# Kernel optimization log

Measured on AMD Instinct MI355X. Metric: run time of the kernel, lower is better.

Reference implementation:

```python
import jax, jax.numpy as jnp
import numpy as np

B = 65536   # batch
D = 48      # despawn feature dim (level*4)
T = 768     # transformer feature dim
F = 512     # fusion_dim
L = 64      # latent_dim
K = 2048    # num_embeddings
H = 4       # attention heads
COMMIT = 0.25


def _ln(x, w, b):
    m = x.mean(-1, keepdims=True)
    v = ((x - m) ** 2).mean(-1, keepdims=True)
    return (x - m) * jax.lax.rsqrt(v + 1e-5) * w + b


def _mha(q, k, v, in_w, in_b, out_w, out_b):
    # torch nn.MultiheadAttention (batch_first), q/k/v: [B, S, F]
    f = q.shape[-1]; dh = f // H
    wq, wk, wv = in_w[:f], in_w[f:2 * f], in_w[2 * f:]
    bq, bk, bv = in_b[:f], in_b[f:2 * f], in_b[2 * f:]
    def proj(x, w, bb):
        y = x @ w.T + bb
        return y.reshape(x.shape[0], x.shape[1], H, dh)
    qh, kh, vh = proj(q, wq, bq), proj(k, wk, bk), proj(v, wv, bv)
    s = jnp.einsum('bqhd,bkhd->bhqk', qh, kh) / jnp.sqrt(jnp.float32(dh))
    a = jax.nn.softmax(s, axis=-1)
    o = jnp.einsum('bhqk,bkhd->bqhd', a, vh).reshape(q.shape[0], q.shape[1], f)
    return o @ out_w.T + out_b


def setup_inputs() -> dict:
    key = jax.random.key(0)
    ks = jax.random.split(key, 32)
    rn = lambda k, s, sc=0.02: jax.random.normal(k, s, jnp.float32) * sc
    return {
        'df': jax.random.normal(ks[0], (B, D), jnp.float32),
        'tf': jax.random.normal(ks[1], (B, T), jnp.float32),
        # HierarchicalFusion params
        'dp_w': rn(ks[2], (F, D)), 'dp_b': jnp.zeros((F,), jnp.float32),
        'tp_w': rn(ks[3], (F, T)), 'tp_b': jnp.zeros((F,), jnp.float32),
        'in_w': rn(ks[4], (3 * F, F)), 'in_b': jnp.zeros((3 * F,), jnp.float32),
        'out_w': rn(ks[5], (F, F)), 'out_b': jnp.zeros((F,), jnp.float32),
        'n1_w': jnp.ones((F,), jnp.float32), 'n1_b': jnp.zeros((F,), jnp.float32),
        'n2_w': jnp.ones((F,), jnp.float32), 'n2_b': jnp.zeros((F,), jnp.float32),
        # encoder: Linear(2F,F) -> LN -> ReLU -> Linear(F,L)
        'e_w1': rn(ks[6], (F, 2 * F)), 'e_b1': jnp.zeros((F,), jnp.float32),
        'e_lnw': jnp.ones((F,), jnp.float32), 'e_lnb': jnp.zeros((F,), jnp.float32),
        'e_w2': rn(ks[7], (L, F)), 'e_b2': jnp.zeros((L,), jnp.float32),
        # VQ codebook, uniform(-1/K, 1/K) as in the module
        'codebook': jax.random.uniform(ks[8], (K, L), jnp.float32, -1.0 / K, 1.0 / K),
        # decoder: Linear(L,F) -> ReLU -> Linear(F,2F)
        'd_w1': rn(ks[9], (F, L)), 'd_b1': jnp.zeros((F,), jnp.float32),
        'd_w2': rn(ks[10], (2 * F, F)), 'd_b2': jnp.zeros((2 * F,), jnp.float32),
    }


def reference(df, tf, dp_w, dp_b, tp_w, tp_b, in_w, in_b, out_w, out_b,
              n1_w, n1_b, n2_w, n2_b, e_w1, e_b1, e_lnw, e_lnb, e_w2, e_b2,
              codebook, d_w1, d_b1, d_w2, d_b2):
    # HierarchicalFusion: project to [B,1,F] tokens, cross-attend both ways
    d = (df @ dp_w.T + dp_b)[:, None, :]
    t = (tf @ tp_w.T + tp_b)[:, None, :]
    d2 = d + _mha(_ln(d, n1_w, n1_b), _ln(t, n1_w, n1_b), _ln(t, n1_w, n1_b),
                  in_w, in_b, out_w, out_b)
    t2 = t + _mha(_ln(t, n2_w, n2_b), _ln(d, n2_w, n2_b), _ln(d, n2_w, n2_b),
                  in_w, in_b, out_w, out_b)
    fused = jnp.concatenate([d2, t2], axis=1).reshape(d2.shape[0], 2 * F)  # [B, 2F]
    # encoder
    h = jax.nn.relu(_ln(fused @ e_w1.T + e_b1, e_lnw, e_lnb)) @ e_w2.T + e_b2  # [B, L]
    # vector quantization: cdist^2 + argmin + gather (equiv to one-hot @ emb)
    dist = (h ** 2).sum(1, keepdims=True) + (codebook ** 2).sum(1) - 2.0 * h @ codebook.T
    idx = jnp.argmin(dist, axis=1)                 # [B]
    quant = codebook[idx]                          # [B, L]
    loss = jnp.mean((jax.lax.stop_gradient(quant) - h) ** 2) + \
           COMMIT * jnp.mean((quant - jax.lax.stop_gradient(h)) ** 2)
    z_q = h + jax.lax.stop_gradient(quant - h)     # straight-through
    # decoder
    rec = jax.nn.relu(z_q @ d_w1.T + d_b1) @ d_w2.T + d_b2  # [B, 2F]
    return rec, loss, idx
```

## Files before the change

### kernel.cpp

```cpp
#include <hip/hip_runtime.h>
#include <math.h>

typedef long long ll;
typedef double f64x4 __attribute__((ext_vector_type(4)));

#define BN 65536LL
#define LOSS_OFF (BN * 1024LL)
#define IDX_OFF  (LOSS_OFF + 1LL)

#define WF_W1 0LL
#define WF_RT (WF_W1 + BN * 512LL)
#define WF_CN (WF_RT + 2048LL * 1024LL)
#define WF_LP (WF_CN + 2048LL)

#define BSTR 522

template<int MODE>
__global__ __launch_bounds__(512, 4)
void k_mmf(const float* __restrict__ A0, const float* __restrict__ A1, int K,
           const float* __restrict__ W, const float* __restrict__ bias,
           const float* __restrict__ resid,
           const float* __restrict__ lnw, const float* __restrict__ lnb,
           float* __restrict__ Y, float* __restrict__ Y2)
{
  __shared__ double As64[16][33];
  __shared__ double pool[4176];
  __shared__ float msh[32], rsh[32];
  float* Bs = (float*)pool;
  double (*red)[65] = (double(*)[65])pool;

  const int tid = threadIdx.x;
  const int w = tid >> 6, l = tid & 63;
  const int q16 = l >> 4, l15 = l & 15;
  const int rbase = (w >> 2) * 16;
  const int cbase = (w & 3) * 128;
  const ll r0 = (ll)blockIdx.x * 32;
  const int strideA0 = A1 ? 512 : K;

  f64x4 acc[8];
#pragma unroll
  for (int f = 0; f < 8; ++f) acc[f] = (f64x4){0.0, 0.0, 0.0, 0.0};

  for (int kc = 0; kc < K; kc += 16) {
    {
      const int row = tid >> 4, k = tid & 15;
      const int cidx = kc + k;
      float v;
      if (A1 && cidx >= 512) v = A1[(r0 + row) * 512LL + (cidx - 512)];
      else                   v = A0[(r0 + row) * (ll)strideA0 + cidx];
      As64[k][row] = (double)v;
    }
#pragma unroll
    for (int m = 0; m < 4; ++m) {
      const int s = m * 512 + tid;
      const int col = s >> 2, kq = s & 3;
      const float4 v = *(const float4*)(W + (ll)col * K + kc + kq * 4);
      Bs[(kq*4+0)*BSTR + col] = v.x;
      Bs[(kq*4+1)*BSTR + col] = v.y;
      Bs[(kq*4+2)*BSTR + col] = v.z;
      Bs[(kq*4+3)*BSTR + col] = v.w;
    }
    __syncthreads();
#pragma unroll
    for (int kq = 0; kq < 4; ++kq) {
      const int kk = kq * 4 + q16;
      const double a = As64[kk][rbase + l15];
#pragma unroll
      for (int f = 0; f < 8; ++f) {
        const double b = (double)Bs[kk * BSTR + cbase + f*16 + l15];
        acc[f] = __builtin_amdgcn_mfma_f64_16x16x4f64(a, b, acc[f], 0, 0, 0);
      }
    }
    __syncthreads();
  }

  float o[8][4];
#pragma unroll
  for (int f = 0; f < 8; ++f)
#pragma unroll
    for (int b = 0; b < 4; ++b) {
      const int row = rbase + q16*4 + b;
      const int col = cbase + f*16 + l15;
      const float mm = (float)acc[f][b];
      const float y1 = mm + bias[col];
      o[f][b] = resid ? (resid[(r0 + row) * 512LL + col] + y1) : y1;
    }

  if (MODE != 2) {
#pragma unroll
    for (int f = 0; f < 8; ++f)
#pragma unroll
      for (int b = 0; b < 4; ++b) {
        const int row = rbase + q16*4 + b;
        const int col = cbase + f*16 + l15;
        Y[(r0 + row) * 512LL + col] = o[f][b];
      }
  }
  if (MODE == 0) return;

#pragma unroll
  for (int b = 0; b < 4; ++b) {
    double s = 0.0;
#pragma unroll
    for (int f = 0; f < 8; ++f) s += (double)o[f][b];
    red[rbase + q16*4 + b][(w & 3) * 16 + l15] = s;
  }
  __syncthreads();
  if (tid < 32) {
    double s = 0.0;
    for (int x = 0; x < 64; ++x) s += red[tid][x];
    msh[tid] = (float)(s * (1.0 / 512.0));
  }
  __syncthreads();
#pragma unroll
  for (int b = 0; b < 4; ++b) {
    const float m32 = msh[rbase + q16*4 + b];
    double s2 = 0.0;
#pragma unroll
    for (int f = 0; f < 8; ++f) {
      o[f][b] = o[f][b] - m32;
      const float sq = o[f][b] * o[f][b];
      s2 += (double)sq;
    }
    red[rbase + q16*4 + b][(w & 3) * 16 + l15] = s2;
  }
  __syncthreads();
  if (tid < 32) {
    double s = 0.0;
    for (int x = 0; x < 64; ++x) s += red[tid][x];
    const float v32 = (float)(s * (1.0 / 512.0));
    const float a32 = v32 + 1e-5f;
    const float sq32 = (float)sqrt((double)a32);
    rsh[tid] = (float)(1.0 / (double)sq32);
  }
  __syncthreads();
  {
    float* dst = (MODE == 1) ? Y2 : Y;
#pragma unroll
    for (int b = 0; b < 4; ++b) {
      const float rs = rsh[rbase + q16*4 + b];
#pragma unroll
      for (int f = 0; f < 8; ++f) {
        const int row = rbase + q16*4 + b;
        const int col = cbase + f*16 + l15;
        float v = ((o[f][b] * rs) * lnw[col]) + lnb[col];
        if (MODE == 2) v = fmaxf(v, 0.f);
        dst[(r0 + row) * 512LL + col] = v;
      }
    }
  }
}

__global__ __launch_bounds__(256)
void k_ln(const float* __restrict__ X, const float* __restrict__ w,
          const float* __restrict__ b, float* __restrict__ Y, int relu)
{
  const int tid = threadIdx.x;
  const int lane = tid & 63, wid = tid >> 6;
  const ll row = (ll)blockIdx.x * 4 + wid;
  const ll base = row * 512;

  float xv[8];
#pragma unroll
  for (int j = 0; j < 8; ++j) xv[j] = X[base + j*64 + lane];

  double s = 0.0;
#pragma unroll
  for (int j = 0; j < 8; ++j) s += (double)xv[j];
#pragma unroll
  for (int off = 32; off > 0; off >>= 1) s += __shfl_down(s, off, 64);
  s = __shfl(s, 0, 64);
  const float m32 = (float)(s * (1.0 / 512.0));

  float xm[8];
  double s2 = 0.0;
#pragma unroll
  for (int j = 0; j < 8; ++j) {
    xm[j] = xv[j] - m32;
    const float sq = xm[j] * xm[j];
    s2 += (double)sq;
  }
#pragma unroll
  for (int off = 32; off > 0; off >>= 1) s2 += __shfl_down(s2, off, 64);
  s2 = __shfl(s2, 0, 64);
  const float v32 = (float)(s2 * (1.0 / 512.0));
  const float a32 = v32 + 1e-5f;
  const float sq32 = (float)sqrt((double)a32);
  const float rs32 = (float)(1.0 / (double)sq32);

#pragma unroll
  for (int j = 0; j < 8; ++j) {
    float o = ((xm[j] * rs32) * w[j*64 + lane]) + b[j*64 + lane];
    if (relu) o = fmaxf(o, 0.f);
    Y[base + j*64 + lane] = o;
  }
}

__global__ __launch_bounds__(256)
void k_pre(const float* __restrict__ cbk, const float* __restrict__ d_w1,
           const float* __restrict__ d_b1, const float* __restrict__ d_w2,
           const float* __restrict__ d_b2,
           float* __restrict__ rect, float* __restrict__ cnorm)
{
  __shared__ float cbs16[16][68];
  __shared__ float pbuf[16][516];
  const int tid = threadIdx.x;
  const int bb = blockIdx.x;

  if (bb < 128) {
    const int e0 = bb * 16;
    {
      const int e = tid >> 4, q = tid & 15;
      const float4 v = *(const float4*)(cbk + (ll)(e0 + e) * 64 + q * 4);
      *(float4*)&cbs16[e][q*4] = v;
    }
    __syncthreads();
    {
      double pa0[16], pa1[16];
#pragma unroll
      for (int e = 0; e < 16; ++e) { pa0[e] = 0.0; pa1[e] = 0.0; }
      const int i0 = tid * 2;
      for (int l = 0; l < 64; l += 4) {
        const float4 w0 = *(const float4*)(d_w1 + (ll)i0 * 64 + l);
        const float4 w1 = *(const float4*)(d_w1 + (ll)(i0 + 1) * 64 + l);
#pragma unroll
        for (int e = 0; e < 16; ++e) {
          const float4 c4 = *(const float4*)&cbs16[e][l];
          pa0[e] = fma((double)w0.x,(double)c4.x, fma((double)w0.y,(double)c4.y,
                   fma((double)w0.z,(double)c4.z, fma((double)w0.w,(double)c4.w, pa0[e]))));
          pa1[e] = fma((double)w1.x,(double)c4.x, fma((double)w1.y,(double)c4.y,
                   fma((double)w1.z,(double)c4.z, fma((double)w1.w,(double)c4.w, pa1[e]))));
        }
      }
      const double db0 = (double)d_b1[i0], db1 = (double)d_b1[i0 + 1];
#pragma unroll
      for (int e = 0; e < 16; ++e) {
        pbuf[e][i0]     = (float)fmax(pa0[e] + db0, 0.0);
        pbuf[e][i0 + 1] = (float)fmax(pa1[e] + db1, 0.0);
      }
    }
    __syncthreads();
    {
      double ra[16][4];
#pragma unroll
      for (int e = 0; e < 16; ++e)
#pragma unroll
        for (int k = 0; k < 4; ++k) ra[e][k] = 0.0;
      const int o4 = tid * 4;
      for (int i4 = 0; i4 < 512; i4 += 4) {
        const float4 w0 = *(const float4*)(d_w2 + (ll)(o4+0) * 512 + i4);
        const float4 w1 = *(const float4*)(d_w2 + (ll)(o4+1) * 512 + i4);
        const float4 w2 = *(const float4*)(d_w2 + (ll)(o4+2) * 512 + i4);
        const float4 w3 = *(const float4*)(d_w2 + (ll)(o4+3) * 512 + i4);
#pragma unroll
        for (int e = 0; e < 16; ++e) {
          const float4 p4 = *(const float4*)&pbuf[e][i4];
          ra[e][0] = fma((double)w0.x,(double)p4.x, fma((double)w0.y,(double)p4.y,
                     fma((double)w0.z,(double)p4.z, fma((double)w0.w,(double)p4.w, ra[e][0]))));
          ra[e][1] = fma((double)w1.x,(double)p4.x, fma((double)w1.y,(double)p4.y,
                     fma((double)w1.z,(double)p4.z, fma((double)w1.w,(double)p4.w, ra[e][1]))));
          ra[e][2] = fma((double)w2.x,(double)p4.x, fma((double)w2.y,(double)p4.y,
                     fma((double)w2.z,(double)p4.z, fma((double)w2.w,(double)p4.w, ra[e][2]))));
          ra[e][3] = fma((double)w3.x,(double)p4.x, fma((double)w3.y,(double)p4.y,
                     fma((double)w3.z,(double)p4.z, fma((double)w3.w,(double)p4.w, ra[e][3]))));
        }
      }
      const float4 db = *(const float4*)(d_b2 + o4);
#pragma unroll
      for (int e = 0; e < 16; ++e) {
        *(float4*)(rect + (ll)(e0 + e) * 1024 + o4) =
          make_float4((float)(ra[e][0]+(double)db.x), (float)(ra[e][1]+(double)db.y),
                      (float)(ra[e][2]+(double)db.z), (float)(ra[e][3]+(double)db.w));
      }
    }
  } else {
    for (int k = tid; k < 2048; k += 256) {
      double s = 0.0;
      for (int l = 0; l < 64; ++l) {
        const float c = cbk[(ll)k * 64 + l];
        const float q = c * c;
        s += (double)q;
      }
      cnorm[k] = (float)s;
    }
  }
}

__global__ __launch_bounds__(256)
void k_head(const float* __restrict__ rin, const float* __restrict__ e_w2,
            const float* __restrict__ e_b2, const float* __restrict__ cbk,
            const float* __restrict__ cnorm, const float* __restrict__ rect,
            float* __restrict__ dout, double* __restrict__ lossP)
{
  __shared__ float As[32][17];
  __shared__ float Bsh[16][68];
  __shared__ float hbuf[32][68];
  __shared__ float hA[32];
  __shared__ float cbs[128][68];
  __shared__ float cns[128];
  __shared__ float redv[32][33];
  __shared__ int   redi[32][33];
  __shared__ int   idxs[32];
  __shared__ double lred[256];
  const int tid = threadIdx.x;
  const int tx = tid & 31, ty = tid >> 5;
  const ll r0 = (ll)blockIdx.x * 32;

  double acc2[4][2];
#pragma unroll
  for (int i = 0; i < 4; ++i) { acc2[i][0] = 0.0; acc2[i][1] = 0.0; }
  for (int kc = 0; kc < 512; kc += 16) {
    if (tid < 128) {
      const int rr = tid >> 2, q = tid & 3;
      const float4 v = *(const float4*)(rin + (r0 + rr) * 512LL + kc + q * 4);
      As[rr][q*4+0] = v.x; As[rr][q*4+1] = v.y; As[rr][q*4+2] = v.z; As[rr][q*4+3] = v.w;
    }
    {
      const int c = tid >> 2, q = tid & 3;
      const float4 v = *(const float4*)(e_w2 + (ll)c * 512 + kc + q * 4);
      Bsh[q*4+0][c] = v.x; Bsh[q*4+1][c] = v.y; Bsh[q*4+2][c] = v.z; Bsh[q*4+3][c] = v.w;
    }
    __syncthreads();
#pragma unroll
    for (int j = 0; j < 16; ++j) {
      const double b0 = (double)Bsh[j][tx*2+0], b1 = (double)Bsh[j][tx*2+1];
      const double a0 = (double)As[ty*4+0][j], a1 = (double)As[ty*4+1][j];
      const double a2 = (double)As[ty*4+2][j], a3 = (double)As[ty*4+3][j];
      acc2[0][0] = fma(a0,b0,acc2[0][0]); acc2[0][1] = fma(a0,b1,acc2[0][1]);
      acc2[1][0] = fma(a1,b0,acc2[1][0]); acc2[1][1] = fma(a1,b1,acc2[1][1]);
      acc2[2][0] = fma(a2,b0,acc2[2][0]); acc2[2][1] = fma(a2,b1,acc2[2][1]);
      acc2[3][0] = fma(a3,b0,acc2[3][0]); acc2[3][1] = fma(a3,b1,acc2[3][1]);
    }
    __syncthreads();
  }
  {
    const float eb0 = e_b2[tx*2+0], eb1 = e_b2[tx*2+1];
#pragma unroll
    for (int i = 0; i < 4; ++i) {
      hbuf[ty*4+i][tx*2+0] = (float)acc2[i][0] + eb0;
      hbuf[ty*4+i][tx*2+1] = (float)acc2[i][1] + eb1;
    }
  }
  __syncthreads();

  if (tid < 32) {
    double s = 0.0;
    for (int l = 0; l < 64; ++l) {
      const float hh = hbuf[tid][l];
      const float q = hh * hh;
      s += (double)q;
    }
    hA[tid] = (float)s;
  }
  __syncthreads();

  float bestv[4]; int besti[4];
#pragma unroll
  for (int i = 0; i < 4; ++i) { bestv[i] = 3.4e38f; besti[i] = 0; }
  for (int c0 = 0; c0 < 2048; c0 += 128) {
#pragma unroll
    for (int m = 0; m < 8; ++m) {
      const int l = m * 256 + tid;
      const int kk = l >> 4, q = l & 15;
      const float4 v = *(const float4*)(cbk + (ll)(c0 + kk) * 64 + q * 4);
      *(float4*)&cbs[kk][q*4] = v;
    }
    if (tid < 128) cns[tid] = cnorm[c0 + tid];
    __syncthreads();
    double dacc[4][4];
#pragma unroll
    for (int i = 0; i < 4; ++i)
#pragma unroll
      for (int j2 = 0; j2 < 4; ++j2) dacc[i][j2] = 0.0;
#pragma unroll
    for (int l = 0; l < 64; l += 4) {
      float4 ha[4], cv[4];
#pragma unroll
      for (int i = 0; i < 4; ++i) ha[i] = *(const float4*)&hbuf[ty*4+i][l];
#pragma unroll
      for (int j2 = 0; j2 < 4; ++j2) cv[j2] = *(const float4*)&cbs[tx + 32*j2][l];
#pragma unroll
      for (int i = 0; i < 4; ++i)
#pragma unroll
        for (int j2 = 0; j2 < 4; ++j2) {
          dacc[i][j2] = fma((double)ha[i].x, (double)cv[j2].x, dacc[i][j2]);
          dacc[i][j2] = fma((double)ha[i].y, (double)cv[j2].y, dacc[i][j2]);
          dacc[i][j2] = fma((double)ha[i].z, (double)cv[j2].z, dacc[i][j2]);
          dacc[i][j2] = fma((double)ha[i].w, (double)cv[j2].w, dacc[i][j2]);
        }
    }
#pragma unroll
    for (int i = 0; i < 4; ++i)
#pragma unroll
      for (int j2 = 0; j2 < 4; ++j2) {
        const float C32 = (float)dacc[i][j2];
        const float D = 2.0f * C32;
        const float E = hA[ty*4+i] + cns[tx + 32*j2];
        const float dist = E - D;
        const int kg = c0 + tx + 32*j2;
        if (dist < bestv[i]) { bestv[i] = dist; besti[i] = kg; }
      }
    __syncthreads();
  }
#pragma unroll
  for (int i = 0; i < 4; ++i) { redv[ty*4+i][tx] = bestv[i]; redi[ty*4+i][tx] = besti[i]; }
  __syncthreads();
  if (tid < 32) {
    float bv = redv[tid][0]; int bi = redi[tid][0];
    for (int x = 1; x < 32; ++x) {
      const float v = redv[tid][x]; const int ii = redi[tid][x];
      if (v < bv || (v == bv && ii < bi)) { bv = v; bi = ii; }
    }
    idxs[tid] = bi;
    dout[IDX_OFF + r0 + tid] = (float)bi;
  }
  __syncthreads();

  {
    const int r = tid >> 3, sl = tid & 7;
    const float* cq = cbk + (ll)idxs[r] * 64 + sl * 8;
    double s = 0.0;
#pragma unroll
    for (int e = 0; e < 8; ++e) {
      const float dx = cq[e] - hbuf[r][sl*8 + e];
      const float sq = dx * dx;
      s += (double)sq;
    }
    lred[tid] = s;
  }
  __syncthreads();
  for (int off = 128; off > 0; off >>= 1) {
    if (tid < off) lred[tid] += lred[tid + off];
    __syncthreads();
  }
  if (tid == 0) lossP[blockIdx.x] = lred[0];

  for (int m = 0; m < 32; ++m) {
    const float4 v = *(const float4*)(rect + (ll)idxs[m] * 1024 + tid * 4);
    *(float4*)(dout + (r0 + m) * 1024 + tid * 4) = v;
  }
}

__global__ __launch_bounds__(256)
void k_loss(const double* __restrict__ lossP, float* __restrict__ dout)
{
  __shared__ double red[256];
  const int tid = threadIdx.x;
  double s = 0.0;
  for (int i = tid; i < 2048; i += 256) s += lossP[i];
  red[tid] = s;
  __syncthreads();
  for (int off = 128; off > 0; off >>= 1) {
    if (tid < off) red[tid] += red[tid + off];
    __syncthreads();
  }
  if (tid == 0) {
    const float m1 = (float)(red[0] * (1.0 / 4194304.0));
    dout[LOSS_OFF] = m1 + 0.25f * m1;
  }
}

extern "C" void kernel_launch(void* const* d_in, const int* in_sizes, int n_in,
                              void* d_out, int out_size, void* d_ws, size_t ws_size,
                              hipStream_t stream)
{
  (void)in_sizes; (void)n_in; (void)out_size; (void)ws_size;
  const float* df    = (const float*)d_in[0];
  const float* tf    = (const float*)d_in[1];
  const float* dp_w  = (const float*)d_in[2];
  const float* dp_b  = (const float*)d_in[3];
  const float* tp_w  = (const float*)d_in[4];
  const float* tp_b  = (const float*)d_in[5];
  const float* in_w  = (const float*)d_in[6];
  const float* in_b  = (const float*)d_in[7];
  const float* out_w = (const float*)d_in[8];
  const float* out_b = (const float*)d_in[9];
  const float* n1w   = (const float*)d_in[10];
  const float* n1b   = (const float*)d_in[11];
  const float* n2w   = (const float*)d_in[12];
  const float* n2b   = (const float*)d_in[13];
  const float* e_w1  = (const float*)d_in[14];
  const float* e_b1  = (const float*)d_in[15];
  const float* e_lnw = (const float*)d_in[16];
  const float* e_lnb = (const float*)d_in[17];
  const float* e_w2  = (const float*)d_in[18];
  const float* e_b2  = (const float*)d_in[19];
  const float* cbk   = (const float*)d_in[20];
  const float* d_w1  = (const float*)d_in[21];
  const float* d_b1  = (const float*)d_in[22];
  const float* d_w2  = (const float*)d_in[23];
  const float* d_b2  = (const float*)d_in[24];
  float* out = (float*)d_out;
  float* ws  = (float*)d_ws;

  float* S0 = out;
  float* S1 = out + BN * 512LL;
  float* S2 = ws + WF_W1;
  float* RT = ws + WF_RT;
  float* CN = ws + WF_CN;
  double* LP = (double*)(ws + WF_LP);

  const float* wv = in_w + 1024LL * 512LL;
  const float* bv = in_b + 1024LL;

  k_pre<<<129, 256, 0, stream>>>(cbk, d_w1, d_b1, d_w2, d_b2, RT, CN);

  k_mmf<1><<<2048, 512, 0, stream>>>(df, nullptr, 48, dp_w, dp_b, nullptr,
                                     n2w, n2b, S0, S1);
  k_mmf<0><<<2048, 512, 0, stream>>>(S1, nullptr, 512, wv, bv, nullptr,
                                     nullptr, nullptr, S1, nullptr);
  k_mmf<0><<<2048, 512, 0, stream>>>(tf, nullptr, 768, tp_w, tp_b, nullptr,
                                     nullptr, nullptr, S2, nullptr);
  k_mmf<0><<<2048, 512, 0, stream>>>(S1, nullptr, 512, out_w, out_b, S2,
                                     nullptr, nullptr, S1, nullptr);
  k_ln<<<16384, 256, 0, stream>>>(S2, n1w, n1b, S2, 0);
  k_mmf<0><<<2048, 512, 0, stream>>>(S2, nullptr, 512, wv, bv, nullptr,
                                     nullptr, nullptr, S2, nullptr);
  k_mmf<0><<<2048, 512, 0, stream>>>(S2, nullptr, 512, out_w, out_b, S0,
                                     nullptr, nullptr, S2, nullptr);
  k_mmf<2><<<2048, 512, 0, stream>>>(S2, S1, 1024, e_w1, e_b1, nullptr,
                                     e_lnw, e_lnb, S2, nullptr);
  k_head<<<2048, 256, 0, stream>>>(S2, e_w2, e_b2, cbk, CN, RT, out, LP);
  k_loss<<<1, 256, 0, stream>>>(LP, out);
}
```

Before: 5.688 ms.

## Double-buffer LDS tiles in fused fp64-MFMA matmul to overlap loads with compute

The K-loop of the fused matmul kernel now uses two LDS buffers for the A and B tiles. Global loads for the next chunk are issued into registers before the MFMA work on the current chunk, then written to the other buffer, so there is one barrier per iteration instead of two. LDS use roughly doubles, about 70KB per block with 512 threads and launch bounds asking for 4 blocks per CU. That may cut occupancy, and it adds register pressure from the prefetched values.

New measurement: 5.202 ms. -8.6%, faster.

```diff
diff --git a/kernel.cpp b/kernel.cpp
--- a/kernel.cpp
+++ b/kernel.cpp
@@ -23,11 +23,10 @@
            const float* __restrict__ lnw, const float* __restrict__ lnb,
            float* __restrict__ Y, float* __restrict__ Y2)
 {
-  __shared__ double As64[16][33];
-  __shared__ double pool[4176];
+  __shared__ double As64[2][16][33];
+  __shared__ double poolB[2][4176];
   __shared__ float msh[32], rsh[32];
-  float* Bs = (float*)pool;
-  double (*red)[65] = (double(*)[65])pool;
+  double (*red)[65] = (double(*)[65])poolB[0];
 
   const int tid = threadIdx.x;
   const int w = tid >> 6, l = tid & 63;
@@ -36,42 +35,79 @@
   const int cbase = (w & 3) * 128;
   const ll r0 = (ll)blockIdx.x * 32;
   const int strideA0 = A1 ? 512 : K;
+  const int arow = tid >> 4, ak = tid & 15;
 
   f64x4 acc[8];
 #pragma unroll
   for (int f = 0; f < 8; ++f) acc[f] = (f64x4){0.0, 0.0, 0.0, 0.0};
 
-  for (int kc = 0; kc < K; kc += 16) {
-    {
-      const int row = tid >> 4, k = tid & 15;
-      const int cidx = kc + k;
-      float v;
-      if (A1 && cidx >= 512) v = A1[(r0 + row) * 512LL + (cidx - 512)];
-      else                   v = A0[(r0 + row) * (ll)strideA0 + cidx];
-      As64[k][row] = (double)v;
-    }
+  {
+    float av = A0[(r0 + arow) * (ll)strideA0 + ak];
+    float4 bv4[4];
 #pragma unroll
     for (int m = 0; m < 4; ++m) {
       const int s = m * 512 + tid;
       const int col = s >> 2, kq = s & 3;
-      const float4 v = *(const float4*)(W + (ll)col * K + kc + kq * 4);
-      Bs[(kq*4+0)*BSTR + col] = v.x;
-      Bs[(kq*4+1)*BSTR + col] = v.y;
-      Bs[(kq*4+2)*BSTR + col] = v.z;
-      Bs[(kq*4+3)*BSTR + col] = v.w;
-    }
-    __syncthreads();
-#pragma unroll
-    for (int kq = 0; kq < 4; ++kq) {
-      const int kk = kq * 4 + q16;
-      const double a = As64[kk][rbase + l15];
-#pragma unroll
-      for (int f = 0; f < 8; ++f) {
-        const double b = (double)Bs[kk * BSTR + cbase + f*16 + l15];
-        acc[f] = __builtin_amdgcn_mfma_f64_16x16x4f64(a, b, acc[f], 0, 0, 0);
-      }
-    }
-    __syncthreads();
+      bv4[m] = *(const float4*)(W + (ll)col * K + kq * 4);
+    }
+    As64[0][ak][arow] = (double)av;
+    float* B0 = (float*)poolB[0];
+#pragma unroll
+    for (int m = 0; m < 4; ++m) {
+      const int s = m * 512 + tid;
+      const int col = s >> 2, kq = s & 3;
+      B0[(kq*4+0)*BSTR + col] = bv4[m].x;
+      B0[(kq*4+1)*BSTR + col] = bv4[m].y;
+      B0[(kq*4+2)*BSTR + col] = bv4[m].z;
+      B0[(kq*4+3)*BSTR + col] = bv4[m].w;
+    }
+  }
+  __syncthreads();
+
+  int cur = 0;
+  for (int kc = 0; kc < K; kc += 16) {
+    const bool more = (kc + 16) < K;
+    float av; float4 bv4[4];
+    if (more) {
+      const int cidx = kc + 16 + ak;
+      if (A1 && cidx >= 512) av = A1[(r0 + arow) * 512LL + (cidx - 512)];
+      else                   av = A0[(r0 + arow) * (ll)strideA0 + cidx];
+#pragma unroll
+      for (int m = 0; m < 4; ++m) {
+        const int s = m * 512 + tid;
+        const int col = s >> 2, kq = s & 3;
+        bv4[m] = *(const float4*)(W + (ll)col * K + kc + 16 + kq * 4);
+      }
+    }
+    {
+      const double (*A_)[33] = As64[cur];
+      const float* B_ = (const float*)poolB[cur];
+#pragma unroll
+      for (int kq = 0; kq < 4; ++kq) {
+        const int kk = kq * 4 + q16;
+        const double a = A_[kk][rbase + l15];
+#pragma unroll
+        for (int f = 0; f < 8; ++f) {
+          const double b = (double)B_[kk * BSTR + cbase + f*16 + l15];
+          acc[f] = __builtin_amdgcn_mfma_f64_16x16x4f64(a, b, acc[f], 0, 0, 0);
+        }
+      }
+    }
+    if (more) {
+      As64[cur ^ 1][ak][arow] = (double)av;
+      float* Bn = (float*)poolB[cur ^ 1];
+#pragma unroll
+      for (int m = 0; m < 4; ++m) {
+        const int s = m * 512 + tid;
+        const int col = s >> 2, kq = s & 3;
+        Bn[(kq*4+0)*BSTR + col] = bv4[m].x;
+        Bn[(kq*4+1)*BSTR + col] = bv4[m].y;
+        Bn[(kq*4+2)*BSTR + col] = bv4[m].z;
+        Bn[(kq*4+3)*BSTR + col] = bv4[m].w;
+      }
+    }
+    __syncthreads();
+    cur ^= 1;
   }
 
   float o[8][4];
```
